# Optimization experiments

Hardware: AMD Instinct MI355X
Metric: run time of the kernel (lower is better)

## Reference

```python
import jax, jax.numpy as jnp
import numpy as np

B, N, D = 64, 1024, 128
K = 6  # hardcoded neighbor count in the module


def setup_inputs() -> dict:
    key = jax.random.key(0)
    ks = jax.random.split(key, 11)
    def lin(k, out_d, in_d):
        kw, kb = jax.random.split(k)
        s = 1.0 / np.sqrt(in_d)
        W = jax.random.uniform(kw, (out_d, in_d), minval=-s, maxval=s, dtype=jnp.float32)
        b = jax.random.uniform(kb, (out_d,), minval=-s, maxval=s, dtype=jnp.float32)
        return W, b
    loc = jax.random.uniform(ks[0], (B, N, 2), dtype=jnp.float32)
    deadline = jax.random.uniform(ks[1], (B, N), dtype=jnp.float32)
    depot = jax.random.uniform(ks[2], (B, 2), dtype=jnp.float32)
    W3d, b3d = lin(ks[3], D, 3)
    W2d, b2d = lin(ks[4], D, 2)
    Wnb, bnb = lin(ks[5], D, K * D)
    Wdep, bdep = lin(ks[6], D, 2)
    return {"loc": loc, "deadline": deadline, "depot": depot,
            "W3d": W3d, "b3d": b3d, "W2d": W2d, "b2d": b2d,
            "Wnb": Wnb, "bnb": bnb, "Wdep": Wdep, "bdep": bdep}


def reference(loc, deadline, depot, W3d, b3d, W2d, b2d, Wnb, bnb, Wdep, bdep):
    x = jnp.concatenate([loc, deadline[:, :, None]], axis=2)  # [B,N,3]
    x2 = x[:, :, 0:2]                                          # [B,N,2]
    F2 = jnp.einsum('bnf,df->bnd', x2, W2d) + b2d              # [B,N,D]
    F3 = jnp.einsum('bnf,df->bnd', x, W3d) + b3d               # [B,N,D]
    # pairwise euclidean distances; indices are non-differentiable -> stop_gradient
    diff = x2[:, None, :, :] - x2[:, :, None, :]               # [B,N,N,2]
    dist = jnp.sqrt(jnp.sum(diff * diff, axis=-1))             # [B,N,N]
    _, neighbors = jax.lax.top_k(jax.lax.stop_gradient(-dist), K)  # [B,N,K] smallest dists (incl. self)
    # faithful quirk: original does F0_embedding_2d[:, neighbors][0] == gather from batch-0 embeddings
    nb = F2[0][neighbors]                                      # [B,N,K,D]
    nb_c = nb.reshape(nb.shape[0], nb.shape[1], K * nb.shape[3])  # [B,N,K*D]
    Fn = jnp.einsum('bnf,df->bnd', nb_c, Wnb) + bnb            # [B,N,D]
    Ff = Fn + F3
    dep = depot @ Wdep.T + bdep                                 # [B,D]
    h = jax.nn.leaky_relu(jnp.concatenate([dep[:, None, :], Ff], axis=1), negative_slope=0.01)
    return h, h.mean(axis=1)
```

## Files before the change

### kernel.cpp

```cpp
#include <hip/hip_runtime.h>
#include <hip/hip_bf16.h>

#define CB 64
#define CN 1024
#define CD 128
#define CK 6

typedef __attribute__((ext_vector_type(8))) short short8;
typedef __attribute__((ext_vector_type(4))) float floatx4;

__device__ __forceinline__ unsigned short f2bf(float f) {
    union { float f; unsigned u; } c; c.f = f;
    unsigned u = c.u;
    u += 0x7FFFu + ((u >> 16) & 1u);
    return (unsigned short)(u >> 16);
}

#define WS_F2B    0
#define WS_WNBB   262144
#define WS_PART   458752
#define WS_NBRS   983040
#define WS_IDS    1769472
#define WS_STARTS 1900544

__global__ void __launch_bounds__(256) k_grid(
    const float* __restrict__ loc,
    const float* __restrict__ W2d,
    const float* __restrict__ b2d,
    const float* __restrict__ Wnb,
    unsigned short* __restrict__ ids,
    int* __restrict__ starts,
    unsigned short* __restrict__ F2b,
    unsigned short* __restrict__ Wnbb)
{
    __shared__ float2 pts[CN];
    __shared__ int cnt[256];
    __shared__ int base[256];
    int b = blockIdx.x, t = threadIdx.x;
    const float2* lb = (const float2*)loc + b * CN;
#pragma unroll
    for (int r = 0; r < 4; ++r) pts[t + r * 256] = lb[t + r * 256];
    cnt[t] = 0;
    __syncthreads();
    int mycell[4];
#pragma unroll
    for (int r = 0; r < 4; ++r) {
        float2 p = pts[t * 4 + r];
        int cx = (int)(p.x * 16.0f); cx = cx > 15 ? 15 : cx;
        int cy = (int)(p.y * 16.0f); cy = cy > 15 ? 15 : cy;
        mycell[r] = (cy << 4) + cx;
        atomicAdd(&cnt[mycell[r]], 1);
    }
    __syncthreads();
    for (int off = 1; off < 256; off <<= 1) {
        int u = (t >= off) ? cnt[t - off] : 0;
        __syncthreads();
        cnt[t] += u;
        __syncthreads();
    }
    int excl = (t == 0) ? 0 : cnt[t - 1];
    base[t] = excl;
    starts[b * 257 + t] = excl;
    if (t == 255) starts[b * 257 + 256] = cnt[255];
    __syncthreads();
#pragma unroll
    for (int r = 0; r < 4; ++r) {
        int pos = atomicAdd(&base[mycell[r]], 1);
        ids[b * CN + pos] = (unsigned short)(t * 4 + r);
    }
#pragma unroll
    for (int e = 0; e < 8; ++e) {
        int idx = b * 2048 + e * 256 + t;
        int n = idx >> 7, d = idx & 127;
        float v = fmaf(loc[n * 2], W2d[d * 2],
                  fmaf(loc[n * 2 + 1], W2d[d * 2 + 1], b2d[d]));
        F2b[idx] = f2bf(v);
    }
#pragma unroll
    for (int e = 0; e < 6; ++e) {
        int idx = b * 1536 + e * 256 + t;
        Wnbb[idx] = f2bf(Wnb[idx]);
    }
}

__global__ void __launch_bounds__(256) k_knn(
    const float* __restrict__ loc,
    const unsigned short* __restrict__ ids,
    const int* __restrict__ starts,
    unsigned short* __restrict__ nbrs)
{
    __shared__ float2 xy_tmp[CN];
    __shared__ float2 xy_s[CN];
    __shared__ unsigned short ids_s[CN];
    __shared__ int st_s[257];
    int t = threadIdx.x;
    int b = blockIdx.x >> 4;
    int qbase = (blockIdx.x & 15) << 6;
    const float2* lb = (const float2*)loc + b * CN;
#pragma unroll
    for (int r = 0; r < 4; ++r) {
        int p = t + r * 256;
        xy_tmp[p] = lb[p];
        ids_s[p] = ids[b * CN + p];
    }
    st_s[t] = starts[b * 257 + t];
    if (t == 0) st_s[256] = starts[b * 257 + 256];
    __syncthreads();
#pragma unroll
    for (int r = 0; r < 4; ++r) {
        int p = t + r * 256;
        xy_s[p] = xy_tmp[ids_s[p]];
    }
    __syncthreads();

    int qp = qbase + (t >> 2);
    int pi = t & 3;
    int q = ids_s[qp];
    float2 qxy = xy_s[qp];
    float xq = qxy.x, yq = qxy.y;
    int cx = (int)(xq * 16.0f); cx = cx > 15 ? 15 : cx;
    int cy = (int)(yq * 16.0f); cy = cy > 15 ? 15 : cy;
    float dk[CK]; int ik[CK];
#pragma unroll
    for (int s = 0; s < CK; ++s) { dk[s] = 1e30f; ik[s] = 0x7FFFFFFF; }
    float dk5sq = __builtin_inff();
    const float h = 0.0625f;

#define KNN_CAND(P)                                                        \
    {                                                                      \
        float2 v = xy_s[P];                                                \
        float dx = __fsub_rn(v.x, xq);                                     \
        float dy = __fsub_rn(v.y, yq);                                     \
        float d2 = __fadd_rn(__fmul_rn(dx, dx), __fmul_rn(dy, dy));        \
        if (d2 < dk5sq) {                                                  \
            float ds = __fsqrt_rn(d2);                                     \
            int j = ids_s[P];                                              \
            if (ds < dk[CK - 1] || (ds == dk[CK - 1] && j < ik[CK - 1])) { \
                float dc = ds; int jc = j;                                 \
                _Pragma("unroll")                                          \
                for (int s = 0; s < CK; ++s) {                             \
                    bool sw = (dc < dk[s]) || (dc == dk[s] && jc < ik[s]); \
                    float od = dk[s]; int oi = ik[s];                      \
                    dk[s] = sw ? dc : od; ik[s] = sw ? jc : oi;            \
                    dc = sw ? od : dc;    jc = sw ? oi : jc;               \
                }                                                          \
                if (ik[CK - 1] != 0x7FFFFFFF)                              \
                    dk5sq = __fmul_rn(dk[CK - 1], dk[CK - 1]) * 1.000001f; \
            }                                                              \
        }                                                                  \
    }

    {
        int yl = cy > 0 ? cy - 1 : 0, yh = cy < 15 ? cy + 1 : 15;
        int xl = cx > 0 ? cx - 1 : 0, xh = cx < 15 ? cx + 1 : 15;
        for (int yy = yl; yy <= yh; ++yy) {
            int p  = st_s[(yy << 4) + xl] + pi;
            int pe = st_s[(yy << 4) + xh + 1];
            for (; p < pe; p += 4) KNN_CAND(p)
        }
    }
    bool done;
    {
        int x0 = cx - 1, x1 = cx + 1, y0 = cy - 1, y1 = cy + 1;
        done = (x0 <= 0 && y0 <= 0 && x1 >= 15 && y1 >= 15);
        float mL = x0 > 0  ? __fsub_rn(xq, (float)x0 * h)       : 1e30f;
        float mR = x1 < 15 ? __fsub_rn((float)(x1 + 1) * h, xq) : 1e30f;
        float mB = y0 > 0  ? __fsub_rn(yq, (float)y0 * h)       : 1e30f;
        float mT = y1 < 15 ? __fsub_rn((float)(y1 + 1) * h, yq) : 1e30f;
        float bound = fminf(fminf(mL, mR), fminf(mB, mT)) * 0.999999f;
        done = done || (ik[CK - 1] != 0x7FFFFFFF && dk[CK - 1] < bound);
    }
    if (!done) {
        for (int r = 2; r < 16; ++r) {
            int x0 = cx - r, x1 = cx + r, y0 = cy - r, y1 = cy + r;
            int yl = y0 < 0 ? 0 : y0, yh = y1 > 15 ? 15 : y1;
            int xl = x0 < 0 ? 0 : x0, xh = x1 > 15 ? 15 : x1;
            for (int yy = yl; yy <= yh; ++yy) {
                bool ey = (yy == y0) || (yy == y1);
                if (ey) {
                    int p  = st_s[(yy << 4) + xl] + pi;
                    int pe = st_s[(yy << 4) + xh + 1];
                    for (; p < pe; p += 4) KNN_CAND(p)
                } else {
                    if (x0 >= 0) {
                        int p  = st_s[(yy << 4) + x0] + pi;
                        int pe = st_s[(yy << 4) + x0 + 1];
                        for (; p < pe; p += 4) KNN_CAND(p)
                    }
                    if (x1 <= 15) {
                        int p  = st_s[(yy << 4) + x1] + pi;
                        int pe = st_s[(yy << 4) + x1 + 1];
                        for (; p < pe; p += 4) KNN_CAND(p)
                    }
                }
            }
            if (x0 <= 0 && y0 <= 0 && x1 >= 15 && y1 >= 15) break;
            float mL = x0 > 0  ? __fsub_rn(xq, (float)x0 * h)       : 1e30f;
            float mR = x1 < 15 ? __fsub_rn((float)(x1 + 1) * h, xq) : 1e30f;
            float mB = y0 > 0  ? __fsub_rn(yq, (float)y0 * h)       : 1e30f;
            float mT = y1 < 15 ? __fsub_rn((float)(y1 + 1) * h, yq) : 1e30f;
            float bound = fminf(fminf(mL, mR), fminf(mB, mT)) * 0.999999f;
            if (ik[CK - 1] != 0x7FFFFFFF && dk[CK - 1] < bound) break;
        }
    }
#undef KNN_CAND

#define KNN_MERGE(MASK)                                                     \
    {                                                                       \
        float od[CK]; int oi[CK];                                           \
        _Pragma("unroll")                                                   \
        for (int s = 0; s < CK; ++s) {                                      \
            od[s] = __shfl_xor(dk[s], MASK);                                \
            oi[s] = __shfl_xor(ik[s], MASK);                                \
        }                                                                   \
        _Pragma("unroll")                                                   \
        for (int e = 0; e < CK; ++e) {                                      \
            float dc = od[e]; int jc = oi[e];                               \
            if ((dc < dk[CK - 1]) || (dc == dk[CK - 1] && jc < ik[CK - 1])) { \
                _Pragma("unroll")                                           \
                for (int s = 0; s < CK; ++s) {                              \
                    bool sw = (dc < dk[s]) || (dc == dk[s] && jc < ik[s]);  \
                    float td = dk[s]; int ti = ik[s];                       \
                    dk[s] = sw ? dc : td; ik[s] = sw ? jc : ti;             \
                    dc = sw ? td : dc;    jc = sw ? ti : jc;                \
                }                                                           \
            }                                                               \
        }                                                                   \
    }
    KNN_MERGE(1)
    KNN_MERGE(2)
#undef KNN_MERGE

    if (pi == 0) {
        unsigned short* o = nbrs + (unsigned)(b * CN + q) * CK;
#pragma unroll
        for (int s = 0; s < CK; ++s) o[s] = (unsigned short)ik[s];
    }
}

__global__ void __launch_bounds__(256) k_gemm(
    const float* __restrict__ loc,
    const float* __restrict__ dl,
    const unsigned short* __restrict__ F2b,
    const unsigned short* __restrict__ Wnbb,
    const unsigned short* __restrict__ nbrs,
    const float* __restrict__ bnb,
    const float* __restrict__ W3d,
    const float* __restrict__ b3d,
    float* __restrict__ outh,
    float* __restrict__ partials)
{
    __shared__ unsigned short As[128 * 40];
    __shared__ unsigned short Bs[128 * 40];
    __shared__ float psum[4][CD];

    int t = threadIdx.x;
    int rowbase = blockIdx.x * 128;
    int bb = rowbase >> 10;

    int ar0 = t >> 2, aseg = t & 3;
    int nb0[CK], nb1[CK];
#pragma unroll
    for (int s = 0; s < CK; ++s) {
        nb0[s] = (int)nbrs[(rowbase + ar0) * CK + s];
        nb1[s] = (int)nbrs[(rowbase + ar0 + 64) * CK + s];
    }

    int wave = t >> 6, lane = t & 63;
    int koff = (lane >> 4) * 8;
    int mrow = lane & 15;
    int bd = t >> 1, bhalf = t & 1;

    floatx4 acc[2][8];
#pragma unroll
    for (int i = 0; i < 2; ++i)
#pragma unroll
        for (int j = 0; j < 8; ++j) acc[i][j] = (floatx4){0.f, 0.f, 0.f, 0.f};

#pragma unroll
    for (int c = 0; c < 24; ++c) {
        const int kk = c >> 2;
        const int inner = (c & 3) * 32;
        __syncthreads();
        *(uint4*)&As[ar0 * 40 + aseg * 8] =
            *(const uint4*)(F2b + nb0[kk] * 128 + inner + aseg * 8);
        *(uint4*)&As[(ar0 + 64) * 40 + aseg * 8] =
            *(const uint4*)(F2b + nb1[kk] * 128 + inner + aseg * 8);
        {
            const uint4* src = (const uint4*)(Wnbb + bd * 768 + c * 32 + bhalf * 16);
            *(uint4*)&Bs[bd * 40 + bhalf * 16] = src[0];
            *(uint4*)&Bs[bd * 40 + bhalf * 16 + 8] = src[1];
        }
        __syncthreads();
        short8 af[2];
#pragma unroll
        for (int i = 0; i < 2; ++i)
            af[i] = *(const short8*)&As[(wave * 32 + i * 16 + mrow) * 40 + koff];
#pragma unroll
        for (int j = 0; j < 8; ++j) {
            short8 bfr = *(const short8*)&Bs[(j * 16 + mrow) * 40 + koff];
#pragma unroll
            for (int i = 0; i < 2; ++i)
                acc[i][j] = __builtin_amdgcn_mfma_f32_16x16x32_bf16(
                    af[i], bfr, acc[i][j], 0, 0, 0);
        }
    }

    int lq = lane >> 4, lc = lane & 15;
    float rl0[8], rl1[8], rdl[8]; int rn[8];
#pragma unroll
    for (int ir = 0; ir < 8; ++ir) {
        int i = ir >> 2, r = ir & 3;
        int mg = rowbase + wave * 32 + i * 16 + lq * 4 + r;
        float2 l2 = ((const float2*)loc)[mg];
        rl0[ir] = l2.x; rl1[ir] = l2.y; rdl[ir] = dl[mg];
        rn[ir] = mg & 1023;
    }
#pragma unroll
    for (int j = 0; j < 8; ++j) {
        int d = j * 16 + lc;
        float w0 = W3d[d * 3], w1 = W3d[d * 3 + 1], w2 = W3d[d * 3 + 2];
        float bias = b3d[d] + bnb[d];
        float csum = 0.f;
#pragma unroll
        for (int ir = 0; ir < 8; ++ir) {
            int i = ir >> 2, r = ir & 3;
            float v = acc[i][j][r] + bias + rl0[ir] * w0 + rl1[ir] * w1 + rdl[ir] * w2;
            float lr = v >= 0.f ? v : 0.01f * v;
            outh[((long)bb * 1025 + rn[ir] + 1) * 128 + d] = lr;
            csum += lr;
        }
        csum += __shfl_xor(csum, 16);
        csum += __shfl_xor(csum, 32);
        if (lq == 0) psum[wave][d] = csum;
    }
    __syncthreads();
    if (t < CD)
        partials[blockIdx.x * 128 + t] =
            psum[0][t] + psum[1][t] + psum[2][t] + psum[3][t];
}

__global__ void k_fin(const float* __restrict__ depot,
                      const float* __restrict__ Wdep,
                      const float* __restrict__ bdep,
                      const float* __restrict__ partials,
                      float* __restrict__ out) {
    int idx = blockIdx.x * 256 + threadIdx.x;
    int b = idx >> 7, d = idx & 127;
    float acc = 0.f;
#pragma unroll
    for (int g = 0; g < 8; ++g) acc += partials[(b * 8 + g) * 128 + d];
    float dv = depot[b * 2] * Wdep[d * 2] + depot[b * 2 + 1] * Wdep[d * 2 + 1] + bdep[d];
    float lr = dv >= 0.f ? dv : 0.01f * dv;
    out[(long)b * 1025 * 128 + d] = lr;
    out[(long)CB * 1025 * 128 + idx] = (acc + lr) * (1.0f / 1025.0f);
}

extern "C" void kernel_launch(void* const* d_in, const int* in_sizes, int n_in,
                              void* d_out, int out_size, void* d_ws, size_t ws_size,
                              hipStream_t stream) {
    const float* loc      = (const float*)d_in[0];
    const float* deadline = (const float*)d_in[1];
    const float* depot    = (const float*)d_in[2];
    const float* W3d      = (const float*)d_in[3];
    const float* b3d      = (const float*)d_in[4];
    const float* W2d      = (const float*)d_in[5];
    const float* b2d      = (const float*)d_in[6];
    const float* Wnb      = (const float*)d_in[7];
    const float* bnb      = (const float*)d_in[8];
    const float* Wdep     = (const float*)d_in[9];
    const float* bdep     = (const float*)d_in[10];
    float* out = (float*)d_out;

    char* ws = (char*)d_ws;
    unsigned short* F2b   = (unsigned short*)(ws + WS_F2B);
    unsigned short* Wnbb  = (unsigned short*)(ws + WS_WNBB);
    float* partials       = (float*)(ws + WS_PART);
    unsigned short* nbrs  = (unsigned short*)(ws + WS_NBRS);
    unsigned short* ids   = (unsigned short*)(ws + WS_IDS);
    int* starts           = (int*)(ws + WS_STARTS);

    k_grid<<<64, 256, 0, stream>>>(loc, W2d, b2d, Wnb, ids, starts, F2b, Wnbb);
    k_knn<<<1024, 256, 0, stream>>>(loc, ids, starts, nbrs);
    k_gemm<<<512, 256, 0, stream>>>(loc, deadline, F2b, Wnbb, nbrs, bnb,
                                    W3d, b3d, out, partials);
    k_fin<<<32, 256, 0, stream>>>(depot, Wdep, bdep, partials, out);
}
```

Baseline: 139.4 us.

## Precompute per-point neighbor projections and replace gathered GEMM with gather-sum

Because neighbors always index batch-0 embeddings, the change precomputes G[m,k,:] = Wnb_k · F2[0][m] once for the 1024 points and all 6 slots, using MFMA in extra blocks of the grid kernel. The per-row GEMM is replaced by a gather kernel that sums six fp32 rows of G and applies the F3 term, LeakyReLU and partial means. This removes the large 65536x768x128 GEMM and its redundant recomputation. In exchange it adds a 3 MB fp32 workspace and scattered reads of G in the gather. Partials are now per 64 rows, so the final kernel sums 16 of them.

```diff
diff --git a/kernel.cpp b/kernel.cpp
--- a/kernel.cpp
+++ b/kernel.cpp
@@ -16,70 +16,148 @@
     return (unsigned short)(u >> 16);
 }
 
-#define WS_F2B    0
-#define WS_WNBB   262144
-#define WS_PART   458752
-#define WS_NBRS   983040
-#define WS_IDS    1769472
-#define WS_STARTS 1900544
-
-__global__ void __launch_bounds__(256) k_grid(
+#define WS_G      0
+#define WS_NBRS   3145728
+#define WS_IDS    3932160
+#define WS_STARTS 4063232
+#define WS_PART   4129024
+
+struct SortSM { float2 pts[CN]; int cnt[256]; int base[256]; };
+struct GSM    { unsigned short As[128 * 40]; unsigned short Bs[128 * 40]; };
+union GridSM  { SortSM s; GSM g; };
+
+__global__ void __launch_bounds__(256) k_gridg(
     const float* __restrict__ loc,
     const float* __restrict__ W2d,
     const float* __restrict__ b2d,
     const float* __restrict__ Wnb,
     unsigned short* __restrict__ ids,
     int* __restrict__ starts,
-    unsigned short* __restrict__ F2b,
-    unsigned short* __restrict__ Wnbb)
+    float* __restrict__ G)
 {
-    __shared__ float2 pts[CN];
-    __shared__ int cnt[256];
-    __shared__ int base[256];
-    int b = blockIdx.x, t = threadIdx.x;
-    const float2* lb = (const float2*)loc + b * CN;
-#pragma unroll
-    for (int r = 0; r < 4; ++r) pts[t + r * 256] = lb[t + r * 256];
-    cnt[t] = 0;
-    __syncthreads();
-    int mycell[4];
-#pragma unroll
-    for (int r = 0; r < 4; ++r) {
-        float2 p = pts[t * 4 + r];
-        int cx = (int)(p.x * 16.0f); cx = cx > 15 ? 15 : cx;
-        int cy = (int)(p.y * 16.0f); cy = cy > 15 ? 15 : cy;
-        mycell[r] = (cy << 4) + cx;
-        atomicAdd(&cnt[mycell[r]], 1);
-    }
-    __syncthreads();
-    for (int off = 1; off < 256; off <<= 1) {
-        int u = (t >= off) ? cnt[t - off] : 0;
+    __shared__ GridSM sm;
+    int t = threadIdx.x;
+
+    if (blockIdx.x < 64) {
+        int b = blockIdx.x;
+        const float2* lb = (const float2*)loc + b * CN;
+#pragma unroll
+        for (int r = 0; r < 4; ++r) sm.s.pts[t + r * 256] = lb[t + r * 256];
+        sm.s.cnt[t] = 0;
         __syncthreads();
-        cnt[t] += u;
+        int mycell[4];
+#pragma unroll
+        for (int r = 0; r < 4; ++r) {
+            float2 p = sm.s.pts[t * 4 + r];
+            int cx = (int)(p.x * 16.0f); cx = cx > 15 ? 15 : cx;
+            int cy = (int)(p.y * 16.0f); cy = cy > 15 ? 15 : cy;
+            mycell[r] = (cy << 4) + cx;
+            atomicAdd(&sm.s.cnt[mycell[r]], 1);
+        }
         __syncthreads();
-    }
-    int excl = (t == 0) ? 0 : cnt[t - 1];
-    base[t] = excl;
-    starts[b * 257 + t] = excl;
-    if (t == 255) starts[b * 257 + 256] = cnt[255];
-    __syncthreads();
-#pragma unroll
-    for (int r = 0; r < 4; ++r) {
-        int pos = atomicAdd(&base[mycell[r]], 1);
-        ids[b * CN + pos] = (unsigned short)(t * 4 + r);
-    }
-#pragma unroll
-    for (int e = 0; e < 8; ++e) {
-        int idx = b * 2048 + e * 256 + t;
-        int n = idx >> 7, d = idx & 127;
-        float v = fmaf(loc[n * 2], W2d[d * 2],
-                  fmaf(loc[n * 2 + 1], W2d[d * 2 + 1], b2d[d]));
-        F2b[idx] = f2bf(v);
-    }
-#pragma unroll
-    for (int e = 0; e < 6; ++e) {
-        int idx = b * 1536 + e * 256 + t;
-        Wnbb[idx] = f2bf(Wnb[idx]);
+        for (int off = 1; off < 256; off <<= 1) {
+            int u = (t >= off) ? sm.s.cnt[t - off] : 0;
+            __syncthreads();
+            sm.s.cnt[t] += u;
+            __syncthreads();
+        }
+        int excl = (t == 0) ? 0 : sm.s.cnt[t - 1];
+        sm.s.base[t] = excl;
+        starts[b * 257 + t] = excl;
+        if (t == 255) starts[b * 257 + 256] = sm.s.cnt[255];
+        __syncthreads();
+#pragma unroll
+        for (int r = 0; r < 4; ++r) {
+            int pos = atomicAdd(&sm.s.base[mycell[r]], 1);
+            ids[b * CN + pos] = (unsigned short)(t * 4 + r);
+        }
+        return;
+    }
+
+    int gb = blockIdx.x - 64;
+    int k = gb % 6;
+    int tile = gb / 6;
+    int n0 = tile << 7;
+
+    int wave = t >> 6, lane = t & 63;
+    int koff = (lane >> 4) * 8;
+    int mrow = lane & 15;
+
+    int e2 = t & 15, rg = t >> 4;
+    float2 pl[8];
+#pragma unroll
+    for (int rr = 0; rr < 8; ++rr)
+        pl[rr] = ((const float2*)loc)[n0 + rg + rr * 16];
+
+    int bd = t >> 1, bhalf = t & 1;
+
+    floatx4 acc[2][8];
+#pragma unroll
+    for (int i = 0; i < 2; ++i)
+#pragma unroll
+        for (int j = 0; j < 8; ++j) acc[i][j] = (floatx4){0.f, 0.f, 0.f, 0.f};
+
+#pragma unroll
+    for (int c = 0; c < 4; ++c) {
+        __syncthreads();
+        {
+            int e0 = c * 32 + e2 * 2;
+            float wx0 = W2d[e0 * 2],     wy0 = W2d[e0 * 2 + 1], bz0 = b2d[e0];
+            float wx1 = W2d[e0 * 2 + 2], wy1 = W2d[e0 * 2 + 3], bz1 = b2d[e0 + 1];
+#pragma unroll
+            for (int rr = 0; rr < 8; ++rr) {
+                float2 p = pl[rr];
+                float v0 = fmaf(p.x, wx0, fmaf(p.y, wy0, bz0));
+                float v1 = fmaf(p.x, wx1, fmaf(p.y, wy1, bz1));
+                unsigned pack = (unsigned)f2bf(v0) | ((unsigned)f2bf(v1) << 16);
+                *(unsigned*)&sm.g.As[(rg + rr * 16) * 40 + e2 * 2] = pack;
+            }
+        }
+        {
+            const float* src = Wnb + bd * 768 + k * 128 + c * 32 + bhalf * 16;
+            float4 f0 = *(const float4*)(src);
+            float4 f1 = *(const float4*)(src + 4);
+            float4 f2v = *(const float4*)(src + 8);
+            float4 f3 = *(const float4*)(src + 12);
+            uint4 o0, o1;
+            o0.x = (unsigned)f2bf(f0.x) | ((unsigned)f2bf(f0.y) << 16);
+            o0.y = (unsigned)f2bf(f0.z) | ((unsigned)f2bf(f0.w) << 16);
+            o0.z = (unsigned)f2bf(f1.x) | ((unsigned)f2bf(f1.y) << 16);
+            o0.w = (unsigned)f2bf(f1.z) | ((unsigned)f2bf(f1.w) << 16);
+            o1.x = (unsigned)f2bf(f2v.x) | ((unsigned)f2bf(f2v.y) << 16);
+            o1.y = (unsigned)f2bf(f2v.z) | ((unsigned)f2bf(f2v.w) << 16);
+            o1.z = (unsigned)f2bf(f3.x) | ((unsigned)f2bf(f3.y) << 16);
+            o1.w = (unsigned)f2bf(f3.z) | ((unsigned)f2bf(f3.w) << 16);
+            *(uint4*)&sm.g.Bs[bd * 40 + bhalf * 16] = o0;
+            *(uint4*)&sm.g.Bs[bd * 40 + bhalf * 16 + 8] = o1;
+        }
+        __syncthreads();
+        short8 af[2];
+#pragma unroll
+        for (int i = 0; i < 2; ++i)
+            af[i] = *(const short8*)&sm.g.As[(wave * 32 + i * 16 + mrow) * 40 + koff];
+#pragma unroll
+        for (int j = 0; j < 8; ++j) {
+            short8 bfr = *(const short8*)&sm.g.Bs[(j * 16 + mrow) * 40 + koff];
+#pragma unroll
+            for (int i = 0; i < 2; ++i)
+                acc[i][j] = __builtin_amdgcn_mfma_f32_16x16x32_bf16(
+                    af[i], bfr, acc[i][j], 0, 0, 0);
+        }
+    }
+
+    int lq = lane >> 4, lc = lane & 15;
+#pragma unroll
+    for (int j = 0; j < 8; ++j) {
+        int d = j * 16 + lc;
+#pragma unroll
+        for (int i = 0; i < 2; ++i) {
+#pragma unroll
+            for (int r = 0; r < 4; ++r) {
+                int row = wave * 32 + i * 16 + lq * 4 + r;
+                G[(n0 + row) * 768 + k * 128 + d] = acc[i][j][r];
+            }
+        }
     }
 }
 
@@ -238,105 +316,75 @@
     }
 }
 
-__global__ void __launch_bounds__(256) k_gemm(
+__global__ void __launch_bounds__(256) k_gather(
     const float* __restrict__ loc,
     const float* __restrict__ dl,
-    const unsigned short* __restrict__ F2b,
-    const unsigned short* __restrict__ Wnbb,
     const unsigned short* __restrict__ nbrs,
-    const float* __restrict__ bnb,
+    const float* __restrict__ G,
     const float* __restrict__ W3d,
     const float* __restrict__ b3d,
+    const float* __restrict__ bnb,
     float* __restrict__ outh,
     float* __restrict__ partials)
 {
-    __shared__ unsigned short As[128 * 40];
-    __shared__ unsigned short Bs[128 * 40];
     __shared__ float psum[4][CD];
-
-    int t = threadIdx.x;
-    int rowbase = blockIdx.x * 128;
-    int bb = rowbase >> 10;
-
-    int ar0 = t >> 2, aseg = t & 3;
-    int nb0[CK], nb1[CK];
-#pragma unroll
-    for (int s = 0; s < CK; ++s) {
-        nb0[s] = (int)nbrs[(rowbase + ar0) * CK + s];
-        nb1[s] = (int)nbrs[(rowbase + ar0 + 64) * CK + s];
-    }
-
+    __shared__ unsigned short nbs[64 * CK];
+    int t = threadIdx.x, bx = blockIdx.x;
+    int rowbase = bx << 6, b = rowbase >> 10;
+
+    if (t < 192)
+        ((unsigned*)nbs)[t] = ((const unsigned*)(nbrs + (size_t)rowbase * CK))[t];
+
+    int d4 = t & 31, rg = t >> 5;
+    int d0 = d4 * 4;
+    float4 w0, w1, w2, bias;
+#pragma unroll
+    for (int dd = 0; dd < 4; ++dd) {
+        int d = d0 + dd;
+        ((float*)&w0)[dd] = W3d[d * 3];
+        ((float*)&w1)[dd] = W3d[d * 3 + 1];
+        ((float*)&w2)[dd] = W3d[d * 3 + 2];
+        ((float*)&bias)[dd] = b3d[d] + bnb[d];
+    }
+    float4 csum = {0.f, 0.f, 0.f, 0.f};
+    __syncthreads();
+
+    for (int rr = 0; rr < 8; ++rr) {
+        int r = rr * 8 + rg;
+        int gr = rowbase + r;
+        const unsigned short* nb = nbs + r * CK;
+        float4 a = {0.f, 0.f, 0.f, 0.f};
+#pragma unroll
+        for (int k2 = 0; k2 < CK; ++k2) {
+            int m = nb[k2];
+            float4 g4 = *(const float4*)(G + m * 768 + k2 * 128 + d0);
+            a.x += g4.x; a.y += g4.y; a.z += g4.z; a.w += g4.w;
+        }
+        float2 l2 = ((const float2*)loc)[gr];
+        float dlv = dl[gr];
+        float4 v;
+        v.x = a.x + bias.x + l2.x * w0.x + l2.y * w1.x + dlv * w2.x;
+        v.y = a.y + bias.y + l2.x * w0.y + l2.y * w1.y + dlv * w2.y;
+        v.z = a.z + bias.z + l2.x * w0.z + l2.y * w1.z + dlv * w2.z;
+        v.w = a.w + bias.w + l2.x * w0.w + l2.y * w1.w + dlv * w2.w;
+        float4 lr;
+        lr.x = v.x >= 0.f ? v.x : 0.01f * v.x;
+        lr.y = v.y >= 0.f ? v.y : 0.01f * v.y;
+        lr.z = v.z >= 0.f ? v.z : 0.01f * v.z;
+        lr.w = v.w >= 0.f ? v.w : 0.01f * v.w;
+        *(float4*)(outh + ((long)b * 1025 + (gr & 1023) + 1) * 128 + d0) = lr;
+        csum.x += lr.x; csum.y += lr.y; csum.z += lr.z; csum.w += lr.w;
+    }
+
+    csum.x += __shfl_xor(csum.x, 32);
+    csum.y += __shfl_xor(csum.y, 32);
+    csum.z += __shfl_xor(csum.z, 32);
+    csum.w += __shfl_xor(csum.w, 32);
     int wave = t >> 6, lane = t & 63;
-    int koff = (lane >> 4) * 8;
-    int mrow = lane & 15;
-    int bd = t >> 1, bhalf = t & 1;
-
-    floatx4 acc[2][8];
-#pragma unroll
-    for (int i = 0; i < 2; ++i)
-#pragma unroll
-        for (int j = 0; j < 8; ++j) acc[i][j] = (floatx4){0.f, 0.f, 0.f, 0.f};
-
-#pragma unroll
-    for (int c = 0; c < 24; ++c) {
-        const int kk = c >> 2;
-        const int inner = (c & 3) * 32;
-        __syncthreads();
-        *(uint4*)&As[ar0 * 40 + aseg * 8] =
-            *(const uint4*)(F2b + nb0[kk] * 128 + inner + aseg * 8);
-        *(uint4*)&As[(ar0 + 64) * 40 + aseg * 8] =
-            *(const uint4*)(F2b + nb1[kk] * 128 + inner + aseg * 8);
-        {
-            const uint4* src = (const uint4*)(Wnbb + bd * 768 + c * 32 + bhalf * 16);
-            *(uint4*)&Bs[bd * 40 + bhalf * 16] = src[0];
-            *(uint4*)&Bs[bd * 40 + bhalf * 16 + 8] = src[1];
-        }
-        __syncthreads();
-        short8 af[2];
-#pragma unroll
-        for (int i = 0; i < 2; ++i)
-            af[i] = *(const short8*)&As[(wave * 32 + i * 16 + mrow) * 40 + koff];
-#pragma unroll
-        for (int j = 0; j < 8; ++j) {
-            short8 bfr = *(const short8*)&Bs[(j * 16 + mrow) * 40 + koff];
-#pragma unroll
-            for (int i = 0; i < 2; ++i)
-                acc[i][j] = __builtin_amdgcn_mfma_f32_16x16x32_bf16(
-                    af[i], bfr, acc[i][j], 0, 0, 0);
-        }
-    }
-
-    int lq = lane >> 4, lc = lane & 15;
-    float rl0[8], rl1[8], rdl[8]; int rn[8];
-#pragma unroll
-    for (int ir = 0; ir < 8; ++ir) {
-        int i = ir >> 2, r = ir & 3;
-        int mg = rowbase + wave * 32 + i * 16 + lq * 4 + r;
-        float2 l2 = ((const float2*)loc)[mg];
-        rl0[ir] = l2.x; rl1[ir] = l2.y; rdl[ir] = dl[mg];
-        rn[ir] = mg & 1023;
-    }
-#pragma unroll
-    for (int j = 0; j < 8; ++j) {
-        int d = j * 16 + lc;
-        float w0 = W3d[d * 3], w1 = W3d[d * 3 + 1], w2 = W3d[d * 3 + 2];
-        float bias = b3d[d] + bnb[d];
-        float csum = 0.f;
-#pragma unroll
-        for (int ir = 0; ir < 8; ++ir) {
-            int i = ir >> 2, r = ir & 3;
-            float v = acc[i][j][r] + bias + rl0[ir] * w0 + rl1[ir] * w1 + rdl[ir] * w2;
-            float lr = v >= 0.f ? v : 0.01f * v;
-            outh[((long)bb * 1025 + rn[ir] + 1) * 128 + d] = lr;
-            csum += lr;
-        }
-        csum += __shfl_xor(csum, 16);
-        csum += __shfl_xor(csum, 32);
-        if (lq == 0) psum[wave][d] = csum;
-    }
+    if (lane < 32) *(float4*)&psum[wave][d0] = csum;
     __syncthreads();
     if (t < CD)
-        partials[blockIdx.x * 128 + t] =
+        partials[(bx << 7) + t] =
             psum[0][t] + psum[1][t] + psum[2][t] + psum[3][t];
 }
 
@@ -349,7 +397,7 @@
     int b = idx >> 7, d = idx & 127;
     float acc = 0.f;
 #pragma unroll
-    for (int g = 0; g < 8; ++g) acc += partials[(b * 8 + g) * 128 + d];
+    for (int g = 0; g < 16; ++g) acc += partials[(b * 16 + g) * 128 + d];
     float dv = depot[b * 2] * Wdep[d * 2] + depot[b * 2 + 1] * Wdep[d * 2 + 1] + bdep[d];
     float lr = dv >= 0.f ? dv : 0.01f * dv;
     out[(long)b * 1025 * 128 + d] = lr;
@@ -373,16 +421,15 @@
     float* out = (float*)d_out;
 
     char* ws = (char*)d_ws;
-    unsigned short* F2b   = (unsigned short*)(ws + WS_F2B);
-    unsigned short* Wnbb  = (unsigned short*)(ws + WS_WNBB);
-    float* partials       = (float*)(ws + WS_PART);
+    float* G              = (float*)(ws + WS_G);
     unsigned short* nbrs  = (unsigned short*)(ws + WS_NBRS);
     unsigned short* ids   = (unsigned short*)(ws + WS_IDS);
     int* starts           = (int*)(ws + WS_STARTS);
-
-    k_grid<<<64, 256, 0, stream>>>(loc, W2d, b2d, Wnb, ids, starts, F2b, Wnbb);
+    float* partials       = (float*)(ws + WS_PART);
+
+    k_gridg<<<112, 256, 0, stream>>>(loc, W2d, b2d, Wnb, ids, starts, G);
     k_knn<<<1024, 256, 0, stream>>>(loc, ids, starts, nbrs);
-    k_gemm<<<512, 256, 0, stream>>>(loc, deadline, F2b, Wnbb, nbrs, bnb,
-                                    W3d, b3d, out, partials);
+    k_gather<<<1024, 256, 0, stream>>>(loc, deadline, nbrs, G, W3d, b3d, bnb,
+                                       out, partials);
     k_fin<<<32, 256, 0, stream>>>(depot, Wdep, bdep, partials, out);
 }
```

New measurement: 136.5 us. 1.02x faster.
